# Kernel tuning notes

Hardware: AMD Instinct MI355X
Metric: run time of the kernel (lower is better)

## Reference

```python
import jax, jax.numpy as jnp
import numpy as np

C = 512
GROUPS = 16
EPS = 1e-6


def group_norm(x, gamma, beta):
    # x: (b, c, h, w)
    b, c, h, w = x.shape
    xg = x.reshape(b, GROUPS, c // GROUPS, h, w)
    mean = xg.mean(axis=(2, 3, 4), keepdims=True)
    var = xg.var(axis=(2, 3, 4), keepdims=True)
    xn = ((xg - mean) * jax.lax.rsqrt(var + EPS)).reshape(b, c, h, w)
    return xn * gamma[None, :, None, None] + beta[None, :, None, None]


def setup_inputs() -> dict:
    key = jax.random.key(0)
    ks = jax.random.split(key, 9)
    scale = 1.0 / np.sqrt(C)
    x = jax.random.normal(ks[0], (32, C, 32, 32), dtype=jnp.float32)
    return {
        "x": x,
        "gn_gamma": jnp.ones((C,), jnp.float32),
        "gn_beta": jnp.zeros((C,), jnp.float32),
        "wq": jax.random.normal(ks[1], (C, C), jnp.float32) * scale,
        "bq": jnp.zeros((C,), jnp.float32),
        "wk": jax.random.normal(ks[2], (C, C), jnp.float32) * scale,
        "bk": jnp.zeros((C,), jnp.float32),
        "wv": jax.random.normal(ks[3], (C, C), jnp.float32) * scale,
        "bv": jnp.zeros((C,), jnp.float32),
        "wp": jax.random.normal(ks[4], (C, C), jnp.float32) * scale,
        "bp": jnp.zeros((C,), jnp.float32),
    }


def reference(x, gn_gamma, gn_beta, wq, bq, wk, bk, wv, bv, wp, bp):
    b, c, h, w = x.shape
    hn = group_norm(x, gn_gamma, gn_beta).reshape(b, c, h * w)  # (b, c, n)
    # 1x1 convs == per-token channel GEMMs
    q = jnp.einsum('oc,bcn->bon', wq, hn) + bq[None, :, None]
    k = jnp.einsum('oc,bcn->bon', wk, hn) + bk[None, :, None]
    v = jnp.einsum('oc,bcn->bon', wv, hn) + bv[None, :, None]
    # scores: (b, n, m) = q^T k, scaled
    s = jnp.einsum('bcn,bcm->bnm', q, k) * (float(c) ** -0.5)
    # original subtracts the global max (shift-invariant) then softmax over dim 2
    s = s - jnp.max(s)
    attn = jax.nn.softmax(s, axis=2)
    # h_ = v @ attn^T  -> (b, c, n)
    out = jnp.einsum('bcm,bnm->bcn', v, attn)
    out = jnp.einsum('oc,bcn->bon', wp, out) + bp[None, :, None]
    return x + out.reshape(b, c, h, w)
```

## Files before the change

### kernel.cpp

```cpp
#include <hip/hip_runtime.h>
#include <hip/hip_bf16.h>

typedef unsigned short u16;
typedef __attribute__((ext_vector_type(8))) short bf16x8;
typedef __attribute__((ext_vector_type(4))) float f32x4;

#define BK 32
#define TILE_ELEMS (128 * BK)

__device__ __forceinline__ u16 f2bf(float f) {
  union { float f; unsigned u; } a; a.f = f;
  unsigned r = a.u + 0x7fffu + ((a.u >> 16) & 1u);
  return (u16)(r >> 16);
}

__device__ __forceinline__ u16 f2h(float f) {
  union { _Float16 h; u16 u; } c; c.h = (_Float16)f; return c.u;
}

__device__ __forceinline__ void stage_async(const u16* __restrict__ g, int ldg,
                                            u16* __restrict__ s, int tid) {
  int lane = tid & 63, wave = tid >> 6;
#pragma unroll
  for (int t = 0; t < 2; ++t) {
    int chunk = (wave * 2 + t) * 64 + lane;
    int row = chunk >> 2, koff = (chunk & 3) << 3;
    __builtin_amdgcn_global_load_lds(
        (const __attribute__((address_space(1))) unsigned int*)(g + (long)row * ldg + koff),
        (__attribute__((address_space(3))) unsigned int*)(s + (wave * 2 + t) * 512),
        16, 0, 0);
  }
}

__device__ __forceinline__ void gemm_core(
    const u16* __restrict__ Ab, const u16* __restrict__ Bb,
    int lda, int ldb, int K, int tid,
    u16* __restrict__ As, u16* __restrict__ Bs, f32x4 (&acc)[4][4]) {
  int wave = tid >> 6, lane = tid & 63;
  int wr = wave >> 1, wc = wave & 1;
  int lrow = lane & 15, quad = lane >> 4;
#pragma unroll
  for (int i = 0; i < 4; ++i)
#pragma unroll
    for (int j = 0; j < 4; ++j) acc[i][j] = (f32x4){0.f, 0.f, 0.f, 0.f};
  stage_async(Ab, lda, As, tid);
  stage_async(Bb, ldb, Bs, tid);
  int cur = 0;
  for (int k0 = 0; k0 < K; k0 += BK) {
    __syncthreads();
    if (k0 + BK < K) {
      stage_async(Ab + k0 + BK, lda, As + (cur ^ 1) * TILE_ELEMS, tid);
      stage_async(Bb + k0 + BK, ldb, Bs + (cur ^ 1) * TILE_ELEMS, tid);
    }
    const u16* Ac = As + cur * TILE_ELEMS;
    const u16* Bc = Bs + cur * TILE_ELEMS;
    bf16x8 af[4], bfr[4];
#pragma unroll
    for (int mt = 0; mt < 4; ++mt)
      af[mt] = *(const bf16x8*)&Ac[(wr * 64 + mt * 16 + lrow) * BK + quad * 8];
#pragma unroll
    for (int nt = 0; nt < 4; ++nt)
      bfr[nt] = *(const bf16x8*)&Bc[(wc * 64 + nt * 16 + lrow) * BK + quad * 8];
#pragma unroll
    for (int mt = 0; mt < 4; ++mt)
#pragma unroll
      for (int nt = 0; nt < 4; ++nt)
        acc[mt][nt] = __builtin_amdgcn_mfma_f32_16x16x32_bf16(af[mt], bfr[nt], acc[mt][nt], 0, 0, 0);
    cur ^= 1;
  }
}

__device__ __forceinline__ void epi_trans_bf16(
    f32x4 (&acc)[4][4], u16* __restrict__ C, long cbase, int m0, int n0, int ldc,
    const float* __restrict__ bias, float scale, int tid) {
  int wave = tid >> 6, lane = tid & 63;
  int wr = wave >> 1, wc = wave & 1;
  int lrow = lane & 15, quad = lane >> 4;
#pragma unroll
  for (int mt = 0; mt < 4; ++mt) {
    int rowbase = m0 + wr * 64 + mt * 16 + quad * 4;
    float4 b4 = bias ? *(const float4*)&bias[rowbase] : make_float4(0.f, 0.f, 0.f, 0.f);
#pragma unroll
    for (int nt = 0; nt < 4; ++nt) {
      int col = n0 + wc * 64 + nt * 16 + lrow;
      f32x4 a = acc[mt][nt];
      uint2 o;
      o.x = (unsigned)f2bf(a[0] * scale + b4.x) | ((unsigned)f2bf(a[1] * scale + b4.y) << 16);
      o.y = (unsigned)f2bf(a[2] * scale + b4.z) | ((unsigned)f2bf(a[3] * scale + b4.w) << 16);
      *(uint2*)(C + cbase + (long)col * ldc + rowbase) = o;
    }
  }
}

template <int MODE>
__global__ __launch_bounds__(256) void gemm_kernel(
    const u16* __restrict__ Ag, const u16* __restrict__ Bg,
    void* __restrict__ C0, void* __restrict__ C1, void* __restrict__ C2,
    const float* __restrict__ bias0, const float* __restrict__ bias1,
    const float* __restrict__ bias2, const float* __restrict__ resid,
    int lda, int ldb, int ldc,
    long strideA, long strideB, long strideC, int K, float scale) {
  __shared__ u16 As[2 * TILE_ELEMS];
  __shared__ u16 Bs[2 * TILE_ELEMS];
  int tid = threadIdx.x;
  int b = blockIdx.z;
  int m0 = blockIdx.y * 128, n0 = blockIdx.x * 128;
  const u16* Ab = Ag + (long)b * strideA + (long)m0 * lda;
  const u16* Bb = Bg + (long)b * strideB + (long)n0 * ldb;
  f32x4 acc[4][4];
  gemm_core(Ab, Bb, lda, ldb, K, tid, As, Bs, acc);

  int wave = tid >> 6, lane = tid & 63;
  int wr = wave >> 1, wc = wave & 1;
  int lrow = lane & 15, quad = lane >> 4;
  long cbase = (long)b * strideC;

  if (MODE == 0) {
    epi_trans_bf16(acc, (u16*)C0, cbase, m0, n0, ldc, bias0, scale, tid);
  } else if (MODE == 1) {
#pragma unroll
    for (int mt = 0; mt < 4; ++mt)
#pragma unroll
      for (int r = 0; r < 4; ++r) {
        int row = m0 + wr * 64 + mt * 16 + quad * 4 + r;
#pragma unroll
        for (int nt = 0; nt < 4; ++nt) {
          int col = n0 + wc * 64 + nt * 16 + lrow;
          ((u16*)C0)[cbase + (long)row * ldc + col] = f2h(acc[mt][nt][r] * scale);
        }
      }
  } else if (MODE == 2) {
#pragma unroll
    for (int mt = 0; mt < 4; ++mt)
#pragma unroll
      for (int r = 0; r < 4; ++r) {
        int row = m0 + wr * 64 + mt * 16 + quad * 4 + r;
        float bv = bias0[row];
#pragma unroll
        for (int nt = 0; nt < 4; ++nt) {
          int col = n0 + wc * 64 + nt * 16 + lrow;
          long idx = cbase + (long)row * ldc + col;
          ((float*)C0)[idx] = acc[mt][nt][r] * scale + bv + resid[idx];
        }
      }
  } else {
    int seg = m0 >> 9;
    int ml = m0 & 511;
    if (seg == 0) {
      epi_trans_bf16(acc, (u16*)C0, cbase, ml, n0, 512, bias0, 1.f, tid);
    } else if (seg == 1) {
      epi_trans_bf16(acc, (u16*)C1, cbase, ml, n0, 512, bias1, 1.f, tid);
    } else {
#pragma unroll
      for (int mt = 0; mt < 4; ++mt)
#pragma unroll
        for (int r = 0; r < 4; ++r) {
          int row = ml + wr * 64 + mt * 16 + quad * 4 + r;
          float bv = bias2[row];
#pragma unroll
          for (int nt = 0; nt < 4; ++nt) {
            int col = n0 + wc * 64 + nt * 16 + lrow;
            ((u16*)C2)[cbase + (long)row * 1024 + col] = f2bf(acc[mt][nt][r] + bv);
          }
        }
    }
  }
}

__global__ __launch_bounds__(256) void groupnorm_kernel(
    const float* __restrict__ x, const float* __restrict__ gamma,
    const float* __restrict__ beta, u16* __restrict__ hnT) {
  int g = blockIdx.x, b = blockIdx.y;
  const float* xb = x + ((long)b * 512 + g * 32) * 1024;
  int tid = threadIdx.x;
  float s = 0.f, sq = 0.f;
  float4 vals[32];
#pragma unroll
  for (int j = 0; j < 32; ++j) {
    float4 v = *(const float4*)(xb + (long)j * 1024 + tid * 4);
    vals[j] = v;
    s += v.x + v.y + v.z + v.w;
    sq += v.x * v.x + v.y * v.y + v.z * v.z + v.w * v.w;
  }
#pragma unroll
  for (int off = 1; off < 64; off <<= 1) {
    s += __shfl_xor(s, off);
    sq += __shfl_xor(sq, off);
  }
  __shared__ float ls[4], lq[4];
  if ((tid & 63) == 0) { ls[tid >> 6] = s; lq[tid >> 6] = sq; }
  __syncthreads();
  float ts = ls[0] + ls[1] + ls[2] + ls[3];
  float tq = lq[0] + lq[1] + lq[2] + lq[3];
  float mean = ts * (1.f / 32768.f);
  float var = tq * (1.f / 32768.f) - mean * mean;
  float rstd = rsqrtf(var + 1e-6f);
  u16* hb = hnT + (long)b * (1024 * 512) + g * 32;
#pragma unroll
  for (int t = 0; t < 4; ++t) {
    u16 row[32];
#pragma unroll
    for (int j = 0; j < 32; ++j) {
      float xv = ((const float*)&vals[j])[t];
      row[j] = f2bf((xv - mean) * rstd * gamma[g * 32 + j] + beta[g * 32 + j]);
    }
    uint4* dst = (uint4*)(hb + (long)(tid * 4 + t) * 512);
    const uint4* src = (const uint4*)row;
    dst[0] = src[0]; dst[1] = src[1]; dst[2] = src[2]; dst[3] = src[3];
  }
}

__global__ __launch_bounds__(256) void softmax_kernel(u16* __restrict__ s) {
  long row = blockIdx.x;
  u16* sr = s + row * 1024;
  int tid = threadIdx.x;
  union { uint2 u; _Float16 h[4]; } c;
  c.u = *(const uint2*)(sr + tid * 4);
  float v0 = (float)c.h[0], v1 = (float)c.h[1], v2 = (float)c.h[2], v3 = (float)c.h[3];
  float m = fmaxf(fmaxf(v0, v1), fmaxf(v2, v3));
#pragma unroll
  for (int off = 1; off < 64; off <<= 1) m = fmaxf(m, __shfl_xor(m, off));
  __shared__ float lm[4], lsum[4];
  if ((tid & 63) == 0) lm[tid >> 6] = m;
  __syncthreads();
  float rowmax = fmaxf(fmaxf(lm[0], lm[1]), fmaxf(lm[2], lm[3]));
  float e0 = expf(v0 - rowmax), e1 = expf(v1 - rowmax);
  float e2 = expf(v2 - rowmax), e3 = expf(v3 - rowmax);
  float sum = e0 + e1 + e2 + e3;
#pragma unroll
  for (int off = 1; off < 64; off <<= 1) sum += __shfl_xor(sum, off);
  if ((tid & 63) == 0) lsum[tid >> 6] = sum;
  __syncthreads();
  float inv = 1.f / (lsum[0] + lsum[1] + lsum[2] + lsum[3]);
  uint2 o;
  o.x = (unsigned)f2bf(e0 * inv) | ((unsigned)f2bf(e1 * inv) << 16);
  o.y = (unsigned)f2bf(e2 * inv) | ((unsigned)f2bf(e3 * inv) << 16);
  *(uint2*)(sr + tid * 4) = o;
}

__global__ __launch_bounds__(256) void convertw_kernel(
    const float* __restrict__ w0, const float* __restrict__ w1,
    const float* __restrict__ w2, const float* __restrict__ w3,
    u16* __restrict__ out) {
  int wsel = blockIdx.x >> 8;
  const float* src = wsel == 0 ? w0 : wsel == 1 ? w1 : wsel == 2 ? w2 : w3;
  int idx = ((blockIdx.x & 255) * 256 + threadIdx.x) * 4;
  float4 v = *(const float4*)(src + idx);
  uint2 o;
  o.x = (unsigned)f2bf(v.x) | ((unsigned)f2bf(v.y) << 16);
  o.y = (unsigned)f2bf(v.z) | ((unsigned)f2bf(v.w) << 16);
  *(uint2*)(out + (long)wsel * 262144 + idx) = o;
}

extern "C" void kernel_launch(void* const* d_in, const int* in_sizes, int n_in,
                              void* d_out, int out_size, void* d_ws, size_t ws_size,
                              hipStream_t stream) {
  const float* x     = (const float*)d_in[0];
  const float* gamma = (const float*)d_in[1];
  const float* beta  = (const float*)d_in[2];
  const float* wq    = (const float*)d_in[3];
  const float* bq    = (const float*)d_in[4];
  const float* wk    = (const float*)d_in[5];
  const float* bk    = (const float*)d_in[6];
  const float* wv    = (const float*)d_in[7];
  const float* bv    = (const float*)d_in[8];
  const float* wp    = (const float*)d_in[9];
  const float* bp    = (const float*)d_in[10];
  float* out = (float*)d_out;
  char* ws = (char*)d_ws;

  u16* wbf = (u16*)ws;
  u16* hnT = (u16*)(ws + (2L << 20));
  u16* qT  = (u16*)(ws + (34L << 20));
  u16* kT  = (u16*)(ws + (66L << 20));
  u16* v   = (u16*)(ws + (98L << 20));
  u16* s16 = (u16*)(ws + (130L << 20));
  u16* aoT = hnT;

  const long SB = 512L * 1024;
  const long SS = 1024L * 1024;
  const float scale = 0.044194173824159216f;

  convertw_kernel<<<1024, 256, 0, stream>>>(wq, wk, wv, wp, wbf);
  groupnorm_kernel<<<dim3(16, 32), 256, 0, stream>>>(x, gamma, beta, hnT);

  gemm_kernel<3><<<dim3(8, 12, 32), 256, 0, stream>>>(
      wbf, hnT, qT, kT, v, bq, bk, bv, nullptr,
      512, 512, 0, 0, SB, SB, 512, 1.f);

  gemm_kernel<1><<<dim3(8, 8, 32), 256, 0, stream>>>(
      qT, kT, s16, nullptr, nullptr, nullptr, nullptr, nullptr, nullptr,
      512, 512, 1024, SB, SB, SS, 512, scale);

  softmax_kernel<<<32 * 1024, 256, 0, stream>>>(s16);

  gemm_kernel<0><<<dim3(8, 4, 32), 256, 0, stream>>>(
      v, s16, aoT, nullptr, nullptr, nullptr, nullptr, nullptr, nullptr,
      1024, 1024, 512, SB, SS, SB, 1024, 1.f);

  gemm_kernel<2><<<dim3(8, 4, 32), 256, 0, stream>>>(
      wbf + 3 * 262144, aoT, out, nullptr, nullptr, bp, nullptr, nullptr, x,
      512, 512, 1024, 0, SB, SB, 512, 1.f);
}
```

Baseline: 423.3 us.

## Use 8-wave GEMM blocks with swizzled LDS and vectorized score epilogue

Doubles GEMM threads per block to 512 (8 waves in a 4x2 grid, each computing 32x64), halving the accumulator count per thread. One async load per thread per stage replaces two. LDS chunks are XOR-rotated by row to cut bank conflicts on fragment reads. The QK^T GEMM swaps operands so its fp16 output can use the transposed, packed 8-byte store instead of scalar 2-byte stores. More waves per CU trade against fewer MFMAs per wave and more barrier participants.

```diff
diff --git a/kernel.cpp b/kernel.cpp
--- a/kernel.cpp
+++ b/kernel.cpp
@@ -6,7 +6,7 @@
 typedef __attribute__((ext_vector_type(4))) float f32x4;
 
 #define BK 32
-#define TILE_ELEMS (128 * BK)
+#define TILE_U16 (128 * BK)
 
 __device__ __forceinline__ u16 f2bf(float f) {
   union { float f; unsigned u; } a; a.f = f;
@@ -21,48 +21,56 @@
 __device__ __forceinline__ void stage_async(const u16* __restrict__ g, int ldg,
                                             u16* __restrict__ s, int tid) {
   int lane = tid & 63, wave = tid >> 6;
-#pragma unroll
-  for (int t = 0; t < 2; ++t) {
-    int chunk = (wave * 2 + t) * 64 + lane;
-    int row = chunk >> 2, koff = (chunk & 3) << 3;
-    __builtin_amdgcn_global_load_lds(
-        (const __attribute__((address_space(1))) unsigned int*)(g + (long)row * ldg + koff),
-        (__attribute__((address_space(3))) unsigned int*)(s + (wave * 2 + t) * 512),
-        16, 0, 0);
-  }
+  int chunk = wave * 64 + lane;
+  int row = chunk >> 2;
+  int kc = (chunk - (row >> 1)) & 3;
+  __builtin_amdgcn_global_load_lds(
+      (const __attribute__((address_space(1))) unsigned int*)(g + (long)row * ldg + kc * 8),
+      (__attribute__((address_space(3))) unsigned int*)(s + wave * 512),
+      16, 0, 0);
 }
 
 __device__ __forceinline__ void gemm_core(
     const u16* __restrict__ Ab, const u16* __restrict__ Bb,
     int lda, int ldb, int K, int tid,
-    u16* __restrict__ As, u16* __restrict__ Bs, f32x4 (&acc)[4][4]) {
-  int wave = tid >> 6, lane = tid & 63;
+    u16* __restrict__ As, u16* __restrict__ Bs, f32x4 (&acc)[2][4]) {
+  int lane = tid & 63, wave = tid >> 6;
   int wr = wave >> 1, wc = wave & 1;
   int lrow = lane & 15, quad = lane >> 4;
-#pragma unroll
-  for (int i = 0; i < 4; ++i)
+  int aoff[2], boff[4];
+#pragma unroll
+  for (int mt = 0; mt < 2; ++mt) {
+    int row = wr * 32 + mt * 16 + lrow;
+    aoff[mt] = row * BK + ((quad + (row >> 1)) & 3) * 8;
+  }
+#pragma unroll
+  for (int nt = 0; nt < 4; ++nt) {
+    int row = wc * 64 + nt * 16 + lrow;
+    boff[nt] = row * BK + ((quad + (row >> 1)) & 3) * 8;
+  }
+#pragma unroll
+  for (int i = 0; i < 2; ++i)
 #pragma unroll
     for (int j = 0; j < 4; ++j) acc[i][j] = (f32x4){0.f, 0.f, 0.f, 0.f};
+
   stage_async(Ab, lda, As, tid);
   stage_async(Bb, ldb, Bs, tid);
   int cur = 0;
   for (int k0 = 0; k0 < K; k0 += BK) {
     __syncthreads();
     if (k0 + BK < K) {
-      stage_async(Ab + k0 + BK, lda, As + (cur ^ 1) * TILE_ELEMS, tid);
-      stage_async(Bb + k0 + BK, ldb, Bs + (cur ^ 1) * TILE_ELEMS, tid);
+      stage_async(Ab + k0 + BK, lda, As + (cur ^ 1) * TILE_U16, tid);
+      stage_async(Bb + k0 + BK, ldb, Bs + (cur ^ 1) * TILE_U16, tid);
     }
-    const u16* Ac = As + cur * TILE_ELEMS;
-    const u16* Bc = Bs + cur * TILE_ELEMS;
-    bf16x8 af[4], bfr[4];
-#pragma unroll
-    for (int mt = 0; mt < 4; ++mt)
-      af[mt] = *(const bf16x8*)&Ac[(wr * 64 + mt * 16 + lrow) * BK + quad * 8];
-#pragma unroll
-    for (int nt = 0; nt < 4; ++nt)
-      bfr[nt] = *(const bf16x8*)&Bc[(wc * 64 + nt * 16 + lrow) * BK + quad * 8];
-#pragma unroll
-    for (int mt = 0; mt < 4; ++mt)
+    const u16* Ac = As + cur * TILE_U16;
+    const u16* Bc = Bs + cur * TILE_U16;
+    bf16x8 af[2], bfr[4];
+#pragma unroll
+    for (int mt = 0; mt < 2; ++mt) af[mt] = *(const bf16x8*)&Ac[aoff[mt]];
+#pragma unroll
+    for (int nt = 0; nt < 4; ++nt) bfr[nt] = *(const bf16x8*)&Bc[boff[nt]];
+#pragma unroll
+    for (int mt = 0; mt < 2; ++mt)
 #pragma unroll
       for (int nt = 0; nt < 4; ++nt)
         acc[mt][nt] = __builtin_amdgcn_mfma_f32_16x16x32_bf16(af[mt], bfr[nt], acc[mt][nt], 0, 0, 0);
@@ -70,71 +78,69 @@
   }
 }
 
-__device__ __forceinline__ void epi_trans_bf16(
-    f32x4 (&acc)[4][4], u16* __restrict__ C, long cbase, int m0, int n0, int ldc,
+template <bool FP16>
+__device__ __forceinline__ void epi_trans(
+    f32x4 (&acc)[2][4], u16* __restrict__ C, long cbase, int m0, int n0, int ldc,
     const float* __restrict__ bias, float scale, int tid) {
-  int wave = tid >> 6, lane = tid & 63;
+  int lane = tid & 63, wave = tid >> 6;
   int wr = wave >> 1, wc = wave & 1;
   int lrow = lane & 15, quad = lane >> 4;
 #pragma unroll
-  for (int mt = 0; mt < 4; ++mt) {
-    int rowbase = m0 + wr * 64 + mt * 16 + quad * 4;
+  for (int mt = 0; mt < 2; ++mt) {
+    int rowbase = m0 + wr * 32 + mt * 16 + quad * 4;
     float4 b4 = bias ? *(const float4*)&bias[rowbase] : make_float4(0.f, 0.f, 0.f, 0.f);
 #pragma unroll
     for (int nt = 0; nt < 4; ++nt) {
       int col = n0 + wc * 64 + nt * 16 + lrow;
       f32x4 a = acc[mt][nt];
+      float v0 = a[0] * scale + b4.x, v1 = a[1] * scale + b4.y;
+      float v2 = a[2] * scale + b4.z, v3 = a[3] * scale + b4.w;
       uint2 o;
-      o.x = (unsigned)f2bf(a[0] * scale + b4.x) | ((unsigned)f2bf(a[1] * scale + b4.y) << 16);
-      o.y = (unsigned)f2bf(a[2] * scale + b4.z) | ((unsigned)f2bf(a[3] * scale + b4.w) << 16);
+      if (FP16) {
+        o.x = (unsigned)f2h(v0) | ((unsigned)f2h(v1) << 16);
+        o.y = (unsigned)f2h(v2) | ((unsigned)f2h(v3) << 16);
+      } else {
+        o.x = (unsigned)f2bf(v0) | ((unsigned)f2bf(v1) << 16);
+        o.y = (unsigned)f2bf(v2) | ((unsigned)f2bf(v3) << 16);
+      }
       *(uint2*)(C + cbase + (long)col * ldc + rowbase) = o;
     }
   }
 }
 
 template <int MODE>
-__global__ __launch_bounds__(256) void gemm_kernel(
+__global__ __launch_bounds__(512, 4) void gemm_kernel(
     const u16* __restrict__ Ag, const u16* __restrict__ Bg,
     void* __restrict__ C0, void* __restrict__ C1, void* __restrict__ C2,
     const float* __restrict__ bias0, const float* __restrict__ bias1,
     const float* __restrict__ bias2, const float* __restrict__ resid,
     int lda, int ldb, int ldc,
     long strideA, long strideB, long strideC, int K, float scale) {
-  __shared__ u16 As[2 * TILE_ELEMS];
-  __shared__ u16 Bs[2 * TILE_ELEMS];
+  __shared__ u16 As[2 * TILE_U16];
+  __shared__ u16 Bs[2 * TILE_U16];
   int tid = threadIdx.x;
   int b = blockIdx.z;
   int m0 = blockIdx.y * 128, n0 = blockIdx.x * 128;
   const u16* Ab = Ag + (long)b * strideA + (long)m0 * lda;
   const u16* Bb = Bg + (long)b * strideB + (long)n0 * ldb;
-  f32x4 acc[4][4];
+  f32x4 acc[2][4];
   gemm_core(Ab, Bb, lda, ldb, K, tid, As, Bs, acc);
 
-  int wave = tid >> 6, lane = tid & 63;
+  int lane = tid & 63, wave = tid >> 6;
   int wr = wave >> 1, wc = wave & 1;
   int lrow = lane & 15, quad = lane >> 4;
   long cbase = (long)b * strideC;
 
   if (MODE == 0) {
-    epi_trans_bf16(acc, (u16*)C0, cbase, m0, n0, ldc, bias0, scale, tid);
+    epi_trans<false>(acc, (u16*)C0, cbase, m0, n0, ldc, bias0, scale, tid);
   } else if (MODE == 1) {
-#pragma unroll
-    for (int mt = 0; mt < 4; ++mt)
+    epi_trans<true>(acc, (u16*)C0, cbase, m0, n0, ldc, nullptr, scale, tid);
+  } else if (MODE == 2) {
+#pragma unroll
+    for (int mt = 0; mt < 2; ++mt)
 #pragma unroll
       for (int r = 0; r < 4; ++r) {
-        int row = m0 + wr * 64 + mt * 16 + quad * 4 + r;
-#pragma unroll
-        for (int nt = 0; nt < 4; ++nt) {
-          int col = n0 + wc * 64 + nt * 16 + lrow;
-          ((u16*)C0)[cbase + (long)row * ldc + col] = f2h(acc[mt][nt][r] * scale);
-        }
-      }
-  } else if (MODE == 2) {
-#pragma unroll
-    for (int mt = 0; mt < 4; ++mt)
-#pragma unroll
-      for (int r = 0; r < 4; ++r) {
-        int row = m0 + wr * 64 + mt * 16 + quad * 4 + r;
+        int row = m0 + wr * 32 + mt * 16 + quad * 4 + r;
         float bv = bias0[row];
 #pragma unroll
         for (int nt = 0; nt < 4; ++nt) {
@@ -147,15 +153,15 @@
     int seg = m0 >> 9;
     int ml = m0 & 511;
     if (seg == 0) {
-      epi_trans_bf16(acc, (u16*)C0, cbase, ml, n0, 512, bias0, 1.f, tid);
+      epi_trans<false>(acc, (u16*)C0, cbase, ml, n0, 512, bias0, 1.f, tid);
     } else if (seg == 1) {
-      epi_trans_bf16(acc, (u16*)C1, cbase, ml, n0, 512, bias1, 1.f, tid);
+      epi_trans<false>(acc, (u16*)C1, cbase, ml, n0, 512, bias1, 1.f, tid);
     } else {
 #pragma unroll
-      for (int mt = 0; mt < 4; ++mt)
+      for (int mt = 0; mt < 2; ++mt)
 #pragma unroll
         for (int r = 0; r < 4; ++r) {
-          int row = ml + wr * 64 + mt * 16 + quad * 4 + r;
+          int row = ml + wr * 32 + mt * 16 + quad * 4 + r;
           float bv = bias2[row];
 #pragma unroll
           for (int nt = 0; nt < 4; ++nt) {
@@ -284,21 +290,21 @@
   convertw_kernel<<<1024, 256, 0, stream>>>(wq, wk, wv, wp, wbf);
   groupnorm_kernel<<<dim3(16, 32), 256, 0, stream>>>(x, gamma, beta, hnT);
 
-  gemm_kernel<3><<<dim3(8, 12, 32), 256, 0, stream>>>(
+  gemm_kernel<3><<<dim3(8, 12, 32), 512, 0, stream>>>(
       wbf, hnT, qT, kT, v, bq, bk, bv, nullptr,
       512, 512, 0, 0, SB, SB, 512, 1.f);
 
-  gemm_kernel<1><<<dim3(8, 8, 32), 256, 0, stream>>>(
-      qT, kT, s16, nullptr, nullptr, nullptr, nullptr, nullptr, nullptr,
+  gemm_kernel<1><<<dim3(8, 8, 32), 512, 0, stream>>>(
+      kT, qT, s16, nullptr, nullptr, nullptr, nullptr, nullptr, nullptr,
       512, 512, 1024, SB, SB, SS, 512, scale);
 
   softmax_kernel<<<32 * 1024, 256, 0, stream>>>(s16);
 
-  gemm_kernel<0><<<dim3(8, 4, 32), 256, 0, stream>>>(
+  gemm_kernel<0><<<dim3(8, 4, 32), 512, 0, stream>>>(
       v, s16, aoT, nullptr, nullptr, nullptr, nullptr, nullptr, nullptr,
       1024, 1024, 512, SB, SS, SB, 1024, 1.f);
 
-  gemm_kernel<2><<<dim3(8, 4, 32), 256, 0, stream>>>(
+  gemm_kernel<2><<<dim3(8, 4, 32), 512, 0, stream>>>(
       wbf + 3 * 262144, aoT, out, nullptr, nullptr, bp, nullptr, nullptr, x,
       512, 512, 1024, 0, SB, SB, 512, 1.f);
 }
```

After: 425.3 us. No clear change (+0.5%).
